# Kernel tuning notes

Hardware: AMD Instinct MI355X
Metric: run time of the kernel (lower is better)

The kernel has to match this reference:

```python
import jax, jax.numpy as jnp
import numpy as np

EMBED_DIM = 1024
NUM_HEADS = 16
HEAD_DIM = EMBED_DIM // NUM_HEADS
WINDOW = 256
B, S = 2, 2048


def setup_inputs() -> dict:
    key = jax.random.key(0)
    ks = jax.random.split(key, 9)
    sc = 1.0 / np.sqrt(EMBED_DIM)
    inp = {
        "x": jax.random.normal(ks[0], (B, S, EMBED_DIM), dtype=jnp.float32),
        "Wq": jax.random.normal(ks[1], (EMBED_DIM, EMBED_DIM), dtype=jnp.float32) * sc,
        "Wk": jax.random.normal(ks[2], (EMBED_DIM, EMBED_DIM), dtype=jnp.float32) * sc,
        "Wv": jax.random.normal(ks[3], (EMBED_DIM, EMBED_DIM), dtype=jnp.float32) * sc,
        "Wo": jax.random.normal(ks[4], (EMBED_DIM, EMBED_DIM), dtype=jnp.float32) * sc,
        "bq": jax.random.normal(ks[5], (EMBED_DIM,), dtype=jnp.float32) * 0.01,
        "bk": jax.random.normal(ks[6], (EMBED_DIM,), dtype=jnp.float32) * 0.01,
        "bv": jax.random.normal(ks[7], (EMBED_DIM,), dtype=jnp.float32) * 0.01,
        "bo": jax.random.normal(ks[8], (EMBED_DIM,), dtype=jnp.float32) * 0.01,
    }
    return inp


def _sliding_window_mask(seq_len: int) -> jnp.ndarray:
    # True where attention is NOT permitted (future or beyond window)
    idx = jnp.arange(seq_len)
    rel = idx[None, :] - idx[:, None]  # (S, S): key_pos - query_pos
    return (rel > 0) | (rel < -WINDOW)


def reference(x, Wq, Wk, Wv, Wo, bq, bk, bv, bo):
    Bx, Sx, E = x.shape
    H, D = NUM_HEADS, HEAD_DIM
    # projections (torch Linear: y = x @ W.T + b)
    q = (x @ Wq.T + bq).reshape(Bx, Sx, H, D).transpose(0, 2, 1, 3)  # (B,H,S,D)
    k = (x @ Wk.T + bk).reshape(Bx, Sx, H, D).transpose(0, 2, 1, 3)
    v = (x @ Wv.T + bv).reshape(Bx, Sx, H, D).transpose(0, 2, 1, 3)
    q = q * (D ** -0.5)
    attn = jnp.einsum("bhqd,bhkd->bhqk", q, k)  # (B,H,S,S) dense scores
    mask = _sliding_window_mask(Sx)
    attn = jnp.where(mask, -jnp.inf, attn)
    attn = jax.nn.softmax(attn, axis=-1)
    y = jnp.einsum("bhqk,bhkd->bhqd", attn, v)
    y = y.transpose(0, 2, 1, 3).reshape(Bx, Sx, E)
    return y @ Wo.T + bo
```

## Files before the change

### kernel.cpp

```cpp
#include <hip/hip_runtime.h>

#define E_DIM 1024
#define NHEAD 16
#define HDIM 64
#define SEQ 2048
#define NBATCH 2
#define WIN 256
#define MTOK (NBATCH * SEQ)
#define BKT 32
#define NT (E_DIM / BKT)

typedef __attribute__((ext_vector_type(4))) float f32x4;
typedef __attribute__((ext_vector_type(8))) short short8;
typedef __attribute__((ext_vector_type(4))) unsigned short u16x4;

#define AS1 __attribute__((address_space(1)))
#define AS3 __attribute__((address_space(3)))

__device__ __forceinline__ void gll16(const void* g, void* l) {
    __builtin_amdgcn_global_load_lds((const AS1 void*)g, (AS3 void*)l, 16, 0, 0);
}

__device__ __forceinline__ unsigned short f2bf(float f) {
    union { float f; unsigned u; } a; a.f = f;
    unsigned r = a.u + 0x7fffu + ((a.u >> 16) & 1u);
    return (unsigned short)(r >> 16);
}

__global__ __launch_bounds__(256) void conv_all(const float* __restrict__ x,
        const float* __restrict__ w0, const float* __restrict__ w1,
        const float* __restrict__ w2, const float* __restrict__ w3,
        unsigned short* __restrict__ xo,
        unsigned short* __restrict__ o0, unsigned short* __restrict__ o1,
        unsigned short* __restrict__ o2, unsigned short* __restrict__ o3) {
    const int seg = blockIdx.y;
    const float* src;
    unsigned short* dst;
    if (seg < 4) { src = x + (size_t)seg * 1048576; dst = xo + (size_t)seg * 1048576; }
    else {
        src = (seg == 4) ? w0 : (seg == 5) ? w1 : (seg == 6) ? w2 : w3;
        dst = (seg == 4) ? o0 : (seg == 5) ? o1 : (seg == 6) ? o2 : o3;
    }
    int i = blockIdx.x * 256 + threadIdx.x;
    float4 v = ((const float4*)src)[i];
    u16x4 o;
    o[0] = f2bf(v.x); o[1] = f2bf(v.y); o[2] = f2bf(v.z); o[3] = f2bf(v.w);
    ((u16x4*)dst)[i] = o;
}

__global__ __launch_bounds__(256, 3) void gemm97_qkv(const unsigned short* __restrict__ xb,
        const unsigned short* __restrict__ wqb, const unsigned short* __restrict__ wkb,
        const unsigned short* __restrict__ wvb,
        const float* __restrict__ bq, const float* __restrict__ bk, const float* __restrict__ bv,
        unsigned short* __restrict__ qo, unsigned short* __restrict__ ko,
        unsigned short* __restrict__ vTo) {
    __shared__ char lds[32768];
    const int tid = threadIdx.x;
    const int w = tid >> 6, l = tid & 63;
    const int r16 = l & 15, kq = l >> 4;
    const int wr = w >> 1, wc = w & 1;
    const int m0 = blockIdx.x * 128;
    const int by = blockIdx.y;
    const int mat = by >> 3;
    const int nb = (by & 7) * 128;
    const unsigned short* Bw = (mat == 0) ? wqb : (mat == 1) ? wkb : wvb;

    const int srow = tid >> 2;
    const int sslot = tid & 3;
    const int fsw = (srow >> 1) & 3;
    const int gslot = (sslot ^ fsw) * 8;
    const unsigned short* aSrc0 = xb + (size_t)(m0 + srow) * E_DIM + gslot;
    const unsigned short* aSrc1 = aSrc0 + (size_t)64 * E_DIM;
    const unsigned short* bSrc0 = Bw + (size_t)(nb + srow) * E_DIM + gslot;
    const unsigned short* bSrc1 = bSrc0 + (size_t)64 * E_DIM;
    const int dstOff = w * 1024;

#define STAGE(t) { char* a_ = lds + ((t) & 1) * 16384 + dstOff; \
                   char* b_ = a_ + 8192; \
                   gll16(aSrc0 + (t) * BKT, a_); gll16(aSrc1 + (t) * BKT, a_ + 4096); \
                   gll16(bSrc0 + (t) * BKT, b_); gll16(bSrc1 + (t) * BKT, b_ + 4096); }

    f32x4 acc[4][4];
    #pragma unroll
    for (int m = 0; m < 4; ++m)
        #pragma unroll
        for (int n = 0; n < 4; ++n)
            acc[m][n] = (f32x4){0.f, 0.f, 0.f, 0.f};

    STAGE(0);

    const int fs = (r16 >> 1) & 3;
    const int rdoff = (kq ^ fs) * 16;

    for (int t = 0; t < NT; ++t) {
        __syncthreads();
        if (t + 1 < NT) STAGE(t + 1);
        char* la = lds + (t & 1) * 16384;
        char* lb = la + 8192;
        short8 af[4], bfr[4];
        #pragma unroll
        for (int m = 0; m < 4; ++m)
            af[m] = *(const short8*)(la + (wr * 64 + m * 16 + r16) * 64 + rdoff);
        #pragma unroll
        for (int n = 0; n < 4; ++n)
            bfr[n] = *(const short8*)(lb + (wc * 64 + n * 16 + r16) * 64 + rdoff);
        __builtin_amdgcn_s_setprio(1);
        #pragma unroll
        for (int m = 0; m < 4; ++m)
            #pragma unroll
            for (int n = 0; n < 4; ++n)
                acc[m][n] = __builtin_amdgcn_mfma_f32_16x16x32_bf16(af[m], bfr[n], acc[m][n], 0, 0, 0);
        __builtin_amdgcn_s_setprio(0);
    }
#undef STAGE

    const float* bias = (mat == 0) ? bq : (mat == 1) ? bk : bv;
    const float scale = (mat == 0) ? 0.125f : 1.0f;
    #pragma unroll
    for (int n = 0; n < 4; ++n) {
        int e = nb + wc * 64 + n * 16 + r16;
        float bb = bias[e];
        int h = e >> 6, d = e & 63;
        #pragma unroll
        for (int m = 0; m < 4; ++m) {
            int tok = m0 + wr * 64 + m * 16 + kq * 4;
            int b = tok >> 11, s = tok & (SEQ - 1);
            if (mat == 2) {
                u16x4 o;
                #pragma unroll
                for (int r = 0; r < 4; ++r) o[r] = f2bf(acc[m][n][r] + bb);
                *(u16x4*)(vTo + ((size_t)(b * NHEAD + h) * HDIM + d) * SEQ + s) = o;
            } else {
                unsigned short* dst = (mat == 0) ? qo : ko;
                #pragma unroll
                for (int r = 0; r < 4; ++r) {
                    float val = (acc[m][n][r] + bb) * scale;
                    dst[((size_t)(b * NHEAD + h) * SEQ + s + r) * HDIM + d] = f2bf(val);
                }
            }
        }
    }
}

__global__ __launch_bounds__(256, 2) void gemm_out(const unsigned short* __restrict__ yb,
        const unsigned short* __restrict__ wob, const float* __restrict__ bo,
        float* __restrict__ out) {
    __shared__ char lds[65536];
    const int tid = threadIdx.x;
    const int w = tid >> 6, l = tid & 63;
    const int r16 = l & 15, kq = l >> 4;
    const int wr = w >> 1, wc = w & 1;
    const int m0 = blockIdx.x * 128;
    const int n0 = blockIdx.y * 128;

    const int srow = tid >> 2;
    const int sslot = tid & 3;
    const int fsw = (srow >> 1) & 3;
    const int gslot = (sslot ^ fsw) * 8;
    const unsigned short* aSrc0 = yb + (size_t)(m0 + srow) * E_DIM + gslot;
    const unsigned short* aSrc1 = aSrc0 + (size_t)64 * E_DIM;
    const unsigned short* bSrc0 = wob + (size_t)(n0 + srow) * E_DIM + gslot;
    const unsigned short* bSrc1 = bSrc0 + (size_t)64 * E_DIM;
    const int dstOff = w * 1024;

#define STAGE_A(t) { char* d_ = lds + ((t) & 3) * 16384 + dstOff; \
                     gll16(aSrc0 + (t) * BKT, d_); gll16(aSrc1 + (t) * BKT, d_ + 4096); }
#define STAGE_B(t) { char* d_ = lds + ((t) & 3) * 16384 + 8192 + dstOff; \
                     gll16(bSrc0 + (t) * BKT, d_); gll16(bSrc1 + (t) * BKT, d_ + 4096); }

    f32x4 acc[4][4];
    #pragma unroll
    for (int m = 0; m < 4; ++m)
        #pragma unroll
        for (int n = 0; n < 4; ++n)
            acc[m][n] = (f32x4){0.f, 0.f, 0.f, 0.f};

    STAGE_A(0); STAGE_B(0); STAGE_A(1); STAGE_B(1);
    asm volatile("s_waitcnt vmcnt(4)" ::: "memory");
    __builtin_amdgcn_sched_barrier(0);
    __builtin_amdgcn_s_barrier();

    const int fs = (r16 >> 1) & 3;
    const int rdoff = (kq ^ fs) * 16;

    for (int t = 0; t < NT; ++t) {
        char* la = lds + (t & 3) * 16384;
        char* lb = la + 8192;
        short8 bfr[4], af[4];
        #pragma unroll
        for (int n = 0; n < 4; ++n)
            bfr[n] = *(const short8*)(lb + (wc * 64 + n * 16 + r16) * 64 + rdoff);
        #pragma unroll
        for (int m = 0; m < 4; ++m)
            af[m] = *(const short8*)(la + (wr * 64 + m * 16 + r16) * 64 + rdoff);
        if (t + 2 < NT) { STAGE_A(t + 2); STAGE_B(t + 2); }
        __builtin_amdgcn_s_barrier();
        asm volatile("s_waitcnt lgkmcnt(0)" ::: "memory");
        __builtin_amdgcn_sched_barrier(0);
        __builtin_amdgcn_s_setprio(1);
        #pragma unroll
        for (int m = 0; m < 4; ++m)
            #pragma unroll
            for (int n = 0; n < 4; ++n)
                acc[m][n] = __builtin_amdgcn_mfma_f32_16x16x32_bf16(af[m], bfr[n], acc[m][n], 0, 0, 0);
        __builtin_amdgcn_s_setprio(0);
        if (t < NT - 1) {
            if (t < NT - 2) { asm volatile("s_waitcnt vmcnt(4)" ::: "memory"); }
            else            { asm volatile("s_waitcnt vmcnt(0)" ::: "memory"); }
            __builtin_amdgcn_sched_barrier(0);
            __builtin_amdgcn_s_barrier();
        }
    }
#undef STAGE_A
#undef STAGE_B

    #pragma unroll
    for (int n = 0; n < 4; ++n) {
        int e = n0 + wc * 64 + n * 16 + r16;
        float bb = bo[e];
        #pragma unroll
        for (int m = 0; m < 4; ++m) {
            #pragma unroll
            for (int r = 0; r < 4; ++r) {
                int tok = m0 + wr * 64 + m * 16 + kq * 4 + r;
                out[(size_t)tok * E_DIM + e] = acc[m][n][r] + bb;
            }
        }
    }
}

template<int MODE, bool PRE>
__device__ __forceinline__ void attn_tile(int k0,
        const unsigned short* __restrict__ kp, const unsigned short* __restrict__ vp,
        int r16, int kq, char* pl,
        const short8 (&qf)[2][2], short8 (&kf)[2][2],
        f32x4 (&po)[2][4], float (&mrow)[2][4], float (&lsum)[2][4]) {
    f32x4 sc[2][2];
    #pragma unroll
    for (int mf = 0; mf < 2; ++mf)
        #pragma unroll
        for (int n = 0; n < 2; ++n) {
            f32x4 z = {0.f, 0.f, 0.f, 0.f};
            z = __builtin_amdgcn_mfma_f32_16x16x32_bf16(qf[mf][0], kf[n][0], z, 0, 0, 0);
            sc[mf][n] = __builtin_amdgcn_mfma_f32_16x16x32_bf16(qf[mf][1], kf[n][1], z, 0, 0, 0);
        }
    if (PRE) {
        #pragma unroll
        for (int n = 0; n < 2; ++n) {
            const unsigned short* kr = kp + (size_t)(k0 + 32 + n * 16 + r16) * HDIM + kq * 8;
            kf[n][0] = *(const short8*)(kr);
            kf[n][1] = *(const short8*)(kr + 32);
        }
    }
    short8 vf[4];
    #pragma unroll
    for (int nn = 0; nn < 4; ++nn)
        vf[nn] = *(const short8*)(vp + (size_t)(nn * 16 + r16) * SEQ + k0 + kq * 8);

    float tmax[2][4];
    #pragma unroll
    for (int mf = 0; mf < 2; ++mf)
        #pragma unroll
        for (int r = 0; r < 4; ++r) {
            int rel = mf * 16 + kq * 4 + r;
            if (MODE == 1) {
                if (r16 < rel)      sc[mf][0][r] = -1e30f;
                if (16 + r16 < rel) sc[mf][1][r] = -1e30f;
            }
            if (MODE == 2) {
                if (r16 > rel)      sc[mf][0][r] = -1e30f;
                if (16 + r16 > rel) sc[mf][1][r] = -1e30f;
            }
            tmax[mf][r] = fmaxf(sc[mf][0][r], sc[mf][1][r]);
        }
    #pragma unroll
    for (int off = 1; off < 16; off <<= 1)
        #pragma unroll
        for (int mf = 0; mf < 2; ++mf)
            #pragma unroll
            for (int r = 0; r < 4; ++r)
                tmax[mf][r] = fmaxf(tmax[mf][r], __shfl_xor(tmax[mf][r], off));
    float pv[2][2][4];
    #pragma unroll
    for (int mf = 0; mf < 2; ++mf)
        #pragma unroll
        for (int r = 0; r < 4; ++r) {
            float mnew = fmaxf(mrow[mf][r], tmax[mf][r]);
            float resc = __expf(mrow[mf][r] - mnew);
            mrow[mf][r] = mnew;
            float p0 = __expf(sc[mf][0][r] - mnew);
            float p1 = __expf(sc[mf][1][r] - mnew);
            lsum[mf][r] = lsum[mf][r] * resc + p0 + p1;
            po[mf][0][r] *= resc; po[mf][1][r] *= resc;
            po[mf][2][r] *= resc; po[mf][3][r] *= resc;
            pv[mf][0][r] = p0; pv[mf][1][r] = p1;
        }
    #pragma unroll
    for (int mf = 0; mf < 2; ++mf)
        #pragma unroll
        for (int r = 0; r < 4; ++r) {
            int row = kq * 4 + r;
            int c0 = r16 ^ ((row & 7) << 3);
            int c1 = c0 ^ 16;
            *(unsigned short*)(pl + mf * 2048 + row * 128 + c0 * 2) = f2bf(pv[mf][0][r]);
            *(unsigned short*)(pl + mf * 2048 + row * 128 + c1 * 2) = f2bf(pv[mf][1][r]);
        }
    short8 pa[2];
    #pragma unroll
    for (int mf = 0; mf < 2; ++mf)
        pa[mf] = *(const short8*)(pl + mf * 2048 + r16 * 128 + ((kq ^ (r16 & 7)) * 16));
    #pragma unroll
    for (int nn = 0; nn < 4; ++nn) {
        po[0][nn] = __builtin_amdgcn_mfma_f32_16x16x32_bf16(pa[0], vf[nn], po[0][nn], 0, 0, 0);
        po[1][nn] = __builtin_amdgcn_mfma_f32_16x16x32_bf16(pa[1], vf[nn], po[1][nn], 0, 0, 0);
    }
}

__global__ __launch_bounds__(256) void attn_swa(const unsigned short* __restrict__ q,
                                                const unsigned short* __restrict__ k,
                                                const unsigned short* __restrict__ vT,
                                                unsigned short* __restrict__ y) {
    __shared__ char plds[4 * 4096];
    const int t = threadIdx.x;
    const int w = t >> 6, l = t & 63;
    const int r16 = l & 15, kq = l >> 4;
    const int wid = blockIdx.x * 4 + w;
    const int bh = wid >> 6;
    const int q0 = (wid & 63) * 32;
    const unsigned short* qp = q + (size_t)bh * SEQ * HDIM;
    const unsigned short* kp = k + (size_t)bh * SEQ * HDIM;
    const unsigned short* vp = vT + (size_t)bh * HDIM * SEQ;
    char* pl = plds + w * 4096;

    short8 qf[2][2];
    #pragma unroll
    for (int mf = 0; mf < 2; ++mf) {
        const unsigned short* qr = qp + (q0 + mf * 16 + r16) * HDIM + kq * 8;
        qf[mf][0] = *(const short8*)(qr);
        qf[mf][1] = *(const short8*)(qr + 32);
    }

    f32x4 po[2][4];
    float mrow[2][4], lsum[2][4];
    #pragma unroll
    for (int mf = 0; mf < 2; ++mf) {
        #pragma unroll
        for (int nn = 0; nn < 4; ++nn) po[mf][nn] = (f32x4){0.f, 0.f, 0.f, 0.f};
        #pragma unroll
        for (int r = 0; r < 4; ++r) { mrow[mf][r] = -1e30f; lsum[mf][r] = 0.f; }
    }

    const int kstart = (q0 >= WIN) ? (q0 - WIN) : 0;
    short8 kf[2][2];
    #pragma unroll
    for (int n = 0; n < 2; ++n) {
        const unsigned short* kr = kp + (size_t)(kstart + n * 16 + r16) * HDIM + kq * 8;
        kf[n][0] = *(const short8*)(kr);
        kf[n][1] = *(const short8*)(kr + 32);
    }

    int k0 = kstart;
    if (q0 >= WIN) {
        attn_tile<1, true>(k0, kp, vp, r16, kq, pl, qf, kf, po, mrow, lsum);
        k0 += 32;
    }
    for (; k0 < q0; k0 += 32)
        attn_tile<0, true>(k0, kp, vp, r16, kq, pl, qf, kf, po, mrow, lsum);
    attn_tile<2, false>(q0, kp, vp, r16, kq, pl, qf, kf, po, mrow, lsum);

    #pragma unroll
    for (int off = 1; off < 16; off <<= 1)
        #pragma unroll
        for (int mf = 0; mf < 2; ++mf)
            #pragma unroll
            for (int r = 0; r < 4; ++r)
                lsum[mf][r] += __shfl_xor(lsum[mf][r], off);

    const int b = bh >> 4, h = bh & 15;
    #pragma unroll
    for (int mf = 0; mf < 2; ++mf)
        #pragma unroll
        for (int nn = 0; nn < 4; ++nn)
            #pragma unroll
            for (int r = 0; r < 4; ++r) {
                int s = q0 + mf * 16 + kq * 4 + r;
                float val = po[mf][nn][r] / lsum[mf][r];
                y[((size_t)(b * SEQ + s)) * E_DIM + h * HDIM + nn * 16 + r16] = f2bf(val);
            }
}

extern "C" void kernel_launch(void* const* d_in, const int* in_sizes, int n_in,
                              void* d_out, int out_size, void* d_ws, size_t ws_size,
                              hipStream_t stream) {
    const float* x  = (const float*)d_in[0];
    const float* Wq = (const float*)d_in[1];
    const float* Wk = (const float*)d_in[2];
    const float* Wv = (const float*)d_in[3];
    const float* Wo = (const float*)d_in[4];
    const float* bq = (const float*)d_in[5];
    const float* bk = (const float*)d_in[6];
    const float* bv = (const float*)d_in[7];
    const float* bo = (const float*)d_in[8];
    float* out = (float*)d_out;

    char* ws = (char*)d_ws;
    unsigned short* xb  = (unsigned short*)(ws);
    unsigned short* wqb = (unsigned short*)(ws + ((size_t)8 << 20));
    unsigned short* wkb = (unsigned short*)(ws + ((size_t)10 << 20));
    unsigned short* wvb = (unsigned short*)(ws + ((size_t)12 << 20));
    unsigned short* wob = (unsigned short*)(ws + ((size_t)14 << 20));
    unsigned short* qw  = (unsigned short*)(ws + ((size_t)16 << 20));
    unsigned short* kw  = (unsigned short*)(ws + ((size_t)24 << 20));
    unsigned short* vTw = (unsigned short*)(ws + ((size_t)40 << 20));
    unsigned short* yw  = (unsigned short*)(ws + ((size_t)48 << 20));

    conv_all<<<dim3(1024, 8), 256, 0, stream>>>(x, Wq, Wk, Wv, Wo, xb, wqb, wkb, wvb, wob);

    gemm97_qkv<<<dim3(32, 24), 256, 0, stream>>>(xb, wqb, wkb, wvb, bq, bk, bv, qw, kw, vTw);
    attn_swa<<<512, 256, 0, stream>>>(qw, kw, vTw, yw);
    gemm_out<<<dim3(32, 8), 256, 0, stream>>>(yw, wob, bo, out);
}
```

Baseline: 164.0 us.

## Store Q/K token-major, transpose V via LDS, shrink output GEMM tiles

The QKV GEMM epilogue now writes Q and K in token-major [B,S,E] layout rather than a per-head layout, so each lane's stores are contiguous across heads. V is transposed through a swizzled LDS tile so the global writes become 16-byte row vectors instead of scattered 8-byte stores. The attention kernel is updated to read Q/K with an E_DIM stride. The output GEMM moves to 128x64 tiles with double buffering and plain __syncthreads, doubling the grid and cutting LDS use, but it drops the deeper hand-tuned pipeline and its waitcnt scheduling.

```diff
diff --git a/kernel.cpp b/kernel.cpp
--- a/kernel.cpp
+++ b/kernel.cpp
@@ -114,44 +114,61 @@
     }
 #undef STAGE
 
+    __syncthreads();
+
     const float* bias = (mat == 0) ? bq : (mat == 1) ? bk : bv;
-    const float scale = (mat == 0) ? 0.125f : 1.0f;
-    #pragma unroll
-    for (int n = 0; n < 4; ++n) {
-        int e = nb + wc * 64 + n * 16 + r16;
-        float bb = bias[e];
-        int h = e >> 6, d = e & 63;
-        #pragma unroll
-        for (int m = 0; m < 4; ++m) {
-            int tok = m0 + wr * 64 + m * 16 + kq * 4;
-            int b = tok >> 11, s = tok & (SEQ - 1);
-            if (mat == 2) {
+    if (mat != 2) {
+        unsigned short* dst = (mat == 0) ? qo : ko;
+        const float scale = (mat == 0) ? 0.125f : 1.0f;
+        #pragma unroll
+        for (int n = 0; n < 4; ++n) {
+            int e = nb + wc * 64 + n * 16 + r16;
+            float bb = bias[e];
+            #pragma unroll
+            for (int m = 0; m < 4; ++m) {
+                int tokb = m0 + wr * 64 + m * 16 + kq * 4;
+                #pragma unroll
+                for (int r = 0; r < 4; ++r)
+                    dst[(size_t)(tokb + r) * E_DIM + e] = f2bf((acc[m][n][r] + bb) * scale);
+            }
+        }
+    } else {
+        char* pl = lds + w * 8192;
+        #pragma unroll
+        for (int n = 0; n < 4; ++n) {
+            int e = nb + wc * 64 + n * 16 + r16;
+            float bb = bias[e];
+            int d = n * 16 + r16;
+            #pragma unroll
+            for (int m = 0; m < 4; ++m) {
+                int s0 = m * 16 + kq * 4;
                 u16x4 o;
                 #pragma unroll
                 for (int r = 0; r < 4; ++r) o[r] = f2bf(acc[m][n][r] + bb);
-                *(u16x4*)(vTo + ((size_t)(b * NHEAD + h) * HDIM + d) * SEQ + s) = o;
-            } else {
-                unsigned short* dst = (mat == 0) ? qo : ko;
-                #pragma unroll
-                for (int r = 0; r < 4; ++r) {
-                    float val = (acc[m][n][r] + bb) * scale;
-                    dst[((size_t)(b * NHEAD + h) * SEQ + s + r) * HDIM + d] = f2bf(val);
-                }
-            }
-        }
+                *(u16x4*)(pl + d * 128 + (((s0 >> 3) ^ (d & 7)) * 16) + (s0 & 7) * 2) = o;
+            }
+        }
+        const int h = (nb + wc * 64) >> 6;
+        const int b = m0 >> 11;
+        const int sbase = (m0 & (SEQ - 1)) + wr * 64;
+        const int dd = l;
+        unsigned short* vrow = vTo + ((size_t)(b * NHEAD + h) * HDIM + dd) * SEQ + sbase;
+        #pragma unroll
+        for (int c = 0; c < 8; ++c)
+            *(short8*)(vrow + c * 8) = *(const short8*)(pl + dd * 128 + ((c ^ (dd & 7)) * 16));
     }
 }
 
 __global__ __launch_bounds__(256, 2) void gemm_out(const unsigned short* __restrict__ yb,
         const unsigned short* __restrict__ wob, const float* __restrict__ bo,
         float* __restrict__ out) {
-    __shared__ char lds[65536];
+    __shared__ char lds[24576];
     const int tid = threadIdx.x;
     const int w = tid >> 6, l = tid & 63;
     const int r16 = l & 15, kq = l >> 4;
     const int wr = w >> 1, wc = w & 1;
     const int m0 = blockIdx.x * 128;
-    const int n0 = blockIdx.y * 128;
+    const int n0 = blockIdx.y * 64;
 
     const int srow = tid >> 2;
     const int sslot = tid & 3;
@@ -160,63 +177,49 @@
     const unsigned short* aSrc0 = yb + (size_t)(m0 + srow) * E_DIM + gslot;
     const unsigned short* aSrc1 = aSrc0 + (size_t)64 * E_DIM;
     const unsigned short* bSrc0 = wob + (size_t)(n0 + srow) * E_DIM + gslot;
-    const unsigned short* bSrc1 = bSrc0 + (size_t)64 * E_DIM;
     const int dstOff = w * 1024;
 
-#define STAGE_A(t) { char* d_ = lds + ((t) & 3) * 16384 + dstOff; \
-                     gll16(aSrc0 + (t) * BKT, d_); gll16(aSrc1 + (t) * BKT, d_ + 4096); }
-#define STAGE_B(t) { char* d_ = lds + ((t) & 3) * 16384 + 8192 + dstOff; \
-                     gll16(bSrc0 + (t) * BKT, d_); gll16(bSrc1 + (t) * BKT, d_ + 4096); }
-
-    f32x4 acc[4][4];
+#define STAGE(t) { char* a_ = lds + ((t) & 1) * 12288 + dstOff; \
+                   gll16(aSrc0 + (t) * BKT, a_); gll16(aSrc1 + (t) * BKT, a_ + 4096); \
+                   gll16(bSrc0 + (t) * BKT, a_ + (8192 - dstOff) + dstOff); }
+
+    f32x4 acc[4][2];
     #pragma unroll
     for (int m = 0; m < 4; ++m)
         #pragma unroll
-        for (int n = 0; n < 4; ++n)
+        for (int n = 0; n < 2; ++n)
             acc[m][n] = (f32x4){0.f, 0.f, 0.f, 0.f};
 
-    STAGE_A(0); STAGE_B(0); STAGE_A(1); STAGE_B(1);
-    asm volatile("s_waitcnt vmcnt(4)" ::: "memory");
-    __builtin_amdgcn_sched_barrier(0);
-    __builtin_amdgcn_s_barrier();
+    STAGE(0);
 
     const int fs = (r16 >> 1) & 3;
     const int rdoff = (kq ^ fs) * 16;
 
     for (int t = 0; t < NT; ++t) {
-        char* la = lds + (t & 3) * 16384;
+        __syncthreads();
+        if (t + 1 < NT) STAGE(t + 1);
+        char* la = lds + (t & 1) * 12288;
         char* lb = la + 8192;
-        short8 bfr[4], af[4];
-        #pragma unroll
-        for (int n = 0; n < 4; ++n)
-            bfr[n] = *(const short8*)(lb + (wc * 64 + n * 16 + r16) * 64 + rdoff);
+        short8 af[4], bfr[2];
         #pragma unroll
         for (int m = 0; m < 4; ++m)
             af[m] = *(const short8*)(la + (wr * 64 + m * 16 + r16) * 64 + rdoff);
-        if (t + 2 < NT) { STAGE_A(t + 2); STAGE_B(t + 2); }
-        __builtin_amdgcn_s_barrier();
-        asm volatile("s_waitcnt lgkmcnt(0)" ::: "memory");
-        __builtin_amdgcn_sched_barrier(0);
+        #pragma unroll
+        for (int n = 0; n < 2; ++n)
+            bfr[n] = *(const short8*)(lb + (wc * 32 + n * 16 + r16) * 64 + rdoff);
         __builtin_amdgcn_s_setprio(1);
         #pragma unroll
         for (int m = 0; m < 4; ++m)
             #pragma unroll
-            for (int n = 0; n < 4; ++n)
+            for (int n = 0; n < 2; ++n)
                 acc[m][n] = __builtin_amdgcn_mfma_f32_16x16x32_bf16(af[m], bfr[n], acc[m][n], 0, 0, 0);
         __builtin_amdgcn_s_setprio(0);
-        if (t < NT - 1) {
-            if (t < NT - 2) { asm volatile("s_waitcnt vmcnt(4)" ::: "memory"); }
-            else            { asm volatile("s_waitcnt vmcnt(0)" ::: "memory"); }
-            __builtin_amdgcn_sched_barrier(0);
-            __builtin_amdgcn_s_barrier();
-        }
-    }
-#undef STAGE_A
-#undef STAGE_B
-
-    #pragma unroll
-    for (int n = 0; n < 4; ++n) {
-        int e = n0 + wc * 64 + n * 16 + r16;
+    }
+#undef STAGE
+
+    #pragma unroll
+    for (int n = 0; n < 2; ++n) {
+        int e = n0 + wc * 32 + n * 16 + r16;
         float bb = bo[e];
         #pragma unroll
         for (int m = 0; m < 4; ++m) {
@@ -247,7 +250,7 @@
     if (PRE) {
         #pragma unroll
         for (int n = 0; n < 2; ++n) {
-            const unsigned short* kr = kp + (size_t)(k0 + 32 + n * 16 + r16) * HDIM + kq * 8;
+            const unsigned short* kr = kp + (size_t)(k0 + 32 + n * 16 + r16) * E_DIM + kq * 8;
             kf[n][0] = *(const short8*)(kr);
             kf[n][1] = *(const short8*)(kr + 32);
         }
@@ -327,15 +330,16 @@
     const int wid = blockIdx.x * 4 + w;
     const int bh = wid >> 6;
     const int q0 = (wid & 63) * 32;
-    const unsigned short* qp = q + (size_t)bh * SEQ * HDIM;
-    const unsigned short* kp = k + (size_t)bh * SEQ * HDIM;
+    const int b = bh >> 4, h = bh & 15;
+    const unsigned short* qp = q + (size_t)b * SEQ * E_DIM + h * HDIM;
+    const unsigned short* kp = k + (size_t)b * SEQ * E_DIM + h * HDIM;
     const unsigned short* vp = vT + (size_t)bh * HDIM * SEQ;
     char* pl = plds + w * 4096;
 
     short8 qf[2][2];
     #pragma unroll
     for (int mf = 0; mf < 2; ++mf) {
-        const unsigned short* qr = qp + (q0 + mf * 16 + r16) * HDIM + kq * 8;
+        const unsigned short* qr = qp + (size_t)(q0 + mf * 16 + r16) * E_DIM + kq * 8;
         qf[mf][0] = *(const short8*)(qr);
         qf[mf][1] = *(const short8*)(qr + 32);
     }
@@ -354,7 +358,7 @@
     short8 kf[2][2];
     #pragma unroll
     for (int n = 0; n < 2; ++n) {
-        const unsigned short* kr = kp + (size_t)(kstart + n * 16 + r16) * HDIM + kq * 8;
+        const unsigned short* kr = kp + (size_t)(kstart + n * 16 + r16) * E_DIM + kq * 8;
         kf[n][0] = *(const short8*)(kr);
         kf[n][1] = *(const short8*)(kr + 32);
     }
@@ -376,7 +380,6 @@
             for (int r = 0; r < 4; ++r)
                 lsum[mf][r] += __shfl_xor(lsum[mf][r], off);
 
-    const int b = bh >> 4, h = bh & 15;
     #pragma unroll
     for (int mf = 0; mf < 2; ++mf)
         #pragma unroll
@@ -418,5 +421,5 @@
 
     gemm97_qkv<<<dim3(32, 24), 256, 0, stream>>>(xb, wqb, wkb, wvb, bq, bk, bv, qw, kw, vTw);
     attn_swa<<<512, 256, 0, stream>>>(qw, kw, vTw, yw);
-    gemm_out<<<dim3(32, 8), 256, 0, stream>>>(yw, wob, bo, out);
-}
+    gemm_out<<<dim3(32, 16), 256, 0, stream>>>(yw, wob, bo, out);
+}
```

Result: no change. 162.8 us (-0.7%).
